# Kernel tuning notes

Measured on AMD Instinct MI355X. Metric: run time of the kernel, lower is better.

## Reference

```python
import jax, jax.numpy as jnp
import numpy as np

N = 100000      # nodes
E = 1600000     # edges (avg degree 16)
D_IN, D_H, D_OUT = 128, 128, 64
NORM_SCALE = 1.0
EPS = 1e-6


def setup_inputs() -> dict:
    key = jax.random.key(0)
    ks = jax.random.split(key, 9)
    x = jax.random.normal(ks[0], (N, D_IN), dtype=jnp.float32)
    edge_index = jax.random.randint(ks[1], (2, E), 0, N, dtype=jnp.int32)
    edge_weight = jax.random.uniform(ks[2], (E,), dtype=jnp.float32)
    # GraphConv = Linear then spmm(adj, .); Glorot-ish init for weights
    W0 = jax.random.normal(ks[3], (D_IN, D_H), dtype=jnp.float32) / np.float32(np.sqrt(D_IN))
    b0 = jnp.zeros((D_H,), jnp.float32)
    W1 = jax.random.normal(ks[4], (D_H, D_H), dtype=jnp.float32) / np.float32(np.sqrt(D_H))
    b1 = jnp.zeros((D_H,), jnp.float32)
    Wout = jax.random.normal(ks[5], (D_H, D_OUT), dtype=jnp.float32) / np.float32(np.sqrt(D_H))
    bout = jnp.zeros((D_OUT,), jnp.float32)
    return {"x": x, "edge_index": edge_index, "edge_weight": edge_weight,
            "W0": W0, "b0": b0, "W1": W1, "b1": b1, "Wout": Wout, "bout": bout}


def _pair_norm(h):
    # PairNorm mode 'PN': center columns, divide by sqrt(mean squared row norm)
    h = h - jnp.mean(h, axis=0, keepdims=True)
    rownorm_mean = jnp.sqrt(EPS + jnp.mean(jnp.sum(h * h, axis=1)))
    return NORM_SCALE * h / rownorm_mean


def reference(x, edge_index, edge_weight, W0, b0, W1, b1, Wout, bout):
    src = edge_index[0]
    dst = edge_index[1]

    def graph_conv(h, W, b):
        h = h @ W + b                              # [N, d_out]
        msg = edge_weight[:, None] * h[src]        # [E, d_out] gather
        return jax.ops.segment_sum(msg, dst, num_segments=N)  # spmm(adj, h)

    x_old = jnp.zeros((), jnp.float32)
    for (W, b) in ((W0, b0), (W1, b1)):
        # dropout p=0 -> identity (omitted)
        h = graph_conv(x, W, b)
        h = jax.nn.relu(_pair_norm(h))
        x = h + x_old        # residual=1 -> skip every layer
        x_old = x
    return graph_conv(x, Wout, bout)
```

## Files before the change

kernel.cpp:

```cpp
#include <hip/hip_runtime.h>

#define N_NODES 100000
#define N_EDGES 1600000
#define DH 128
#define DOUT 64
#define EPS 1e-6f
#define NBINS 8
#define BINW 12500
#define NREP 64

__device__ inline unsigned bfround(float f) {
    unsigned u = __float_as_uint(f);
    return (u + 0x7fffu + ((u >> 16) & 1u)) >> 16;
}
__device__ inline unsigned pack2(float a, float b) { return bfround(a) | (bfround(b) << 16); }

template <int COLS, int PN, bool OUTBF>
__global__ __launch_bounds__(256) void gemm_kernel(const float* __restrict__ Xa,
                                                   const float* __restrict__ muA,
                                                   const float* __restrict__ invA,
                                                   const float* __restrict__ Xb,
                                                   const float* __restrict__ muB,
                                                   const float* __restrict__ invB,
                                                   const float* __restrict__ W,
                                                   const float* __restrict__ bias,
                                                   void* __restrict__ Yv, int nrows) {
    constexpr int K = 128;
    constexpr int BK = 64;
    constexpr int COLG = COLS / 8;
    constexpr int ROWG = 256 / COLG;
    constexpr int RPT = 64 / ROWG;

    __shared__ float wlds[BK * COLS];
    __shared__ float xlds[64][BK + 1];

    const int tid = threadIdx.x;
    const int row0 = blockIdx.x * 64;

    const float sA = (PN >= 1) ? invA[0] : 0.f;
    const float sB = (PN == 2) ? invB[0] : 0.f;

    const int colg = tid % COLG;
    const int rowg = tid / COLG;
    const int c0 = colg * 8;
    const int r0 = rowg * RPT;

    float acc[RPT][8];
#pragma unroll
    for (int i = 0; i < RPT; ++i)
#pragma unroll
        for (int j = 0; j < 8; ++j) acc[i][j] = 0.f;

    for (int kb = 0; kb < K; kb += BK) {
        constexpr int WVEC = BK * COLS / 4;
        for (int i = tid; i < WVEC; i += 256) {
            int kr = i / (COLS / 4);
            int c4 = i % (COLS / 4);
            reinterpret_cast<float4*>(wlds)[i] =
                reinterpret_cast<const float4*>(W)[(size_t)(kb + kr) * (COLS / 4) + c4];
        }
        for (int i = tid; i < 64 * (BK / 4); i += 256) {
            int r = i / (BK / 4);
            int c4 = i % (BK / 4);
            int col4 = kb / 4 + c4;
            float4 v = make_float4(0.f, 0.f, 0.f, 0.f);
            if (row0 + r < nrows) {
                v = reinterpret_cast<const float4*>(Xa + (size_t)(row0 + r) * K)[col4];
                if constexpr (PN >= 1) {
                    float4 m = reinterpret_cast<const float4*>(muA)[col4];
                    v.x = fmaxf((v.x - m.x) * sA, 0.f);
                    v.y = fmaxf((v.y - m.y) * sA, 0.f);
                    v.z = fmaxf((v.z - m.z) * sA, 0.f);
                    v.w = fmaxf((v.w - m.w) * sA, 0.f);
                }
                if constexpr (PN == 2) {
                    float4 v2 = reinterpret_cast<const float4*>(Xb + (size_t)(row0 + r) * K)[col4];
                    float4 m2 = reinterpret_cast<const float4*>(muB)[col4];
                    v.x += fmaxf((v2.x - m2.x) * sB, 0.f);
                    v.y += fmaxf((v2.y - m2.y) * sB, 0.f);
                    v.z += fmaxf((v2.z - m2.z) * sB, 0.f);
                    v.w += fmaxf((v2.w - m2.w) * sB, 0.f);
                }
            }
            xlds[r][c4 * 4 + 0] = v.x;
            xlds[r][c4 * 4 + 1] = v.y;
            xlds[r][c4 * 4 + 2] = v.z;
            xlds[r][c4 * 4 + 3] = v.w;
        }
        __syncthreads();

        for (int k = 0; k < BK; ++k) {
            float4 w0 = *reinterpret_cast<const float4*>(&wlds[k * COLS + c0]);
            float4 w1 = *reinterpret_cast<const float4*>(&wlds[k * COLS + c0 + 4]);
#pragma unroll
            for (int i = 0; i < RPT; ++i) {
                float xv = xlds[r0 + i][k];
                acc[i][0] += xv * w0.x;
                acc[i][1] += xv * w0.y;
                acc[i][2] += xv * w0.z;
                acc[i][3] += xv * w0.w;
                acc[i][4] += xv * w1.x;
                acc[i][5] += xv * w1.y;
                acc[i][6] += xv * w1.z;
                acc[i][7] += xv * w1.w;
            }
        }
        __syncthreads();
    }

    float bv[8];
#pragma unroll
    for (int j = 0; j < 8; ++j) bv[j] = bias[c0 + j];

#pragma unroll
    for (int i = 0; i < RPT; ++i) {
        int row = row0 + r0 + i;
        if (row < nrows) {
#pragma unroll
            for (int j = 0; j < 8; ++j) acc[i][j] += bv[j];
            if constexpr (OUTBF) {
                uint4 q;
                q.x = pack2(acc[i][0], acc[i][1]);
                q.y = pack2(acc[i][2], acc[i][3]);
                q.z = pack2(acc[i][4], acc[i][5]);
                q.w = pack2(acc[i][6], acc[i][7]);
                *reinterpret_cast<uint4*>((unsigned*)Yv + ((size_t)row * COLS + c0) / 2) = q;
            } else {
                float4 o0 = make_float4(acc[i][0], acc[i][1], acc[i][2], acc[i][3]);
                float4 o1 = make_float4(acc[i][4], acc[i][5], acc[i][6], acc[i][7]);
                float4* yp = reinterpret_cast<float4*>((float*)Yv + (size_t)row * COLS + c0);
                yp[0] = o0;
                yp[1] = o1;
            }
        }
    }
}

__global__ __launch_bounds__(256) void hist_kernel(const int* __restrict__ dst,
                                                   int* __restrict__ counts) {
    int e = blockIdx.x * blockDim.x + threadIdx.x;
    const int stride = gridDim.x * blockDim.x;
    for (; e < N_EDGES; e += stride) atomicAdd(&counts[dst[e]], 1);
}

__global__ __launch_bounds__(1024) void scan_kernel(const int* __restrict__ counts,
                                                    int* __restrict__ rowptr) {
    __shared__ int wsum[16];
    const int tid = threadIdx.x;
    const int lane = tid & 63;
    const int w = tid >> 6;
    int offset = 0;
    if (tid == 0) rowptr[0] = 0;
    for (int base = 0; base < N_NODES; base += 4096) {
        int i = base + tid * 4;
        int4 v = make_int4(0, 0, 0, 0);
        if (i < N_NODES) v = *reinterpret_cast<const int4*>(counts + i);
        int p0 = v.x, p1 = p0 + v.y, p2 = p1 + v.z, p3 = p2 + v.w;
        int incl = p3;
#pragma unroll
        for (int d = 1; d < 64; d <<= 1) {
            int t = __shfl_up(incl, d, 64);
            if (lane >= d) incl += t;
        }
        if (lane == 63) wsum[w] = incl;
        __syncthreads();
        if (w == 0 && lane < 16) {
            int t = wsum[lane];
#pragma unroll
            for (int d = 1; d < 16; d <<= 1) {
                int u = __shfl_up(t, d, 64);
                if (lane >= d) t += u;
            }
            wsum[lane] = t;
        }
        __syncthreads();
        int woff = (w == 0) ? 0 : wsum[w - 1];
        int chunk_total = wsum[15];
        int tbase = offset + woff + incl - p3;
        if (i < N_NODES) {
            rowptr[i + 1] = tbase + p0;
            rowptr[i + 2] = tbase + p1;
            rowptr[i + 3] = tbase + p2;
            rowptr[i + 4] = tbase + p3;
        }
        offset += chunk_total;
        __syncthreads();
    }
}

__global__ __launch_bounds__(256) void bucket_kernel(const int* __restrict__ src,
                                                     const int* __restrict__ dst,
                                                     const float* __restrict__ ew,
                                                     const int* __restrict__ rowptr,
                                                     int* __restrict__ fill,
                                                     int2* __restrict__ em) {
    const int myBin = blockIdx.x & (NBINS - 1);
    const int lo = myBin * BINW;
    const int hi = lo + BINW;
    int e = (blockIdx.x >> 3) * 256 + threadIdx.x;
    const int stride = (gridDim.x >> 3) * 256;
    for (; e < N_EDGES; e += stride) {
        int d = dst[e];
        if (d >= lo && d < hi) {
            int pos = atomicAdd(&fill[d], 1);
            em[rowptr[d] + pos] = make_int2(src[e], __float_as_int(ew[e]));
        }
    }
}

__global__ __launch_bounds__(256) void agg128b_kernel(const unsigned* __restrict__ Hb,
                                                      const int* __restrict__ rowptr,
                                                      const int2* __restrict__ em,
                                                      float* __restrict__ B,
                                                      float* __restrict__ cs_part,
                                                      float* __restrict__ ss_part) {
    __shared__ float cs[4][128];
    __shared__ float ssw[4];
    const int wv = threadIdx.x >> 6;
    const int lane = threadIdx.x & 63;
    const int node = blockIdx.x * 4 + wv;
    const int beg = rowptr[node];
    const int end = rowptr[node + 1];
    float2 acc = make_float2(0.f, 0.f);
    for (int c = beg; c < end; c += 64) {
        int2 m = (c + lane < end) ? em[c + lane] : make_int2(0, 0);
        const int cnt = min(64, end - c);
        int k = 0;
        for (; k + 4 <= cnt; k += 4) {
#pragma unroll
            for (int j = 0; j < 4; ++j) {
                int s = __shfl(m.x, k + j, 64);
                float w = __int_as_float(__shfl(m.y, k + j, 64));
                unsigned u = Hb[(size_t)s * 64 + lane];
                acc.x += w * __uint_as_float(u << 16);
                acc.y += w * __uint_as_float(u & 0xffff0000u);
            }
        }
        for (; k < cnt; ++k) {
            int s = __shfl(m.x, k, 64);
            float w = __int_as_float(__shfl(m.y, k, 64));
            unsigned u = Hb[(size_t)s * 64 + lane];
            acc.x += w * __uint_as_float(u << 16);
            acc.y += w * __uint_as_float(u & 0xffff0000u);
        }
    }
    reinterpret_cast<float2*>(B + (size_t)node * DH)[lane] = acc;

    cs[wv][lane * 2] = acc.x;
    cs[wv][lane * 2 + 1] = acc.y;
    float sq = acc.x * acc.x + acc.y * acc.y;
#pragma unroll
    for (int off = 32; off; off >>= 1) sq += __shfl_down(sq, off, 64);
    if (lane == 0) ssw[wv] = sq;
    __syncthreads();
    const int rep = blockIdx.x & (NREP - 1);
    if (threadIdx.x < 128) {
        float s = cs[0][threadIdx.x] + cs[1][threadIdx.x] + cs[2][threadIdx.x] + cs[3][threadIdx.x];
        atomicAdd(&cs_part[rep * 128 + threadIdx.x], s);
    }
    if (threadIdx.x == 0) atomicAdd(&ss_part[rep], ssw[0] + ssw[1] + ssw[2] + ssw[3]);
}

__global__ __launch_bounds__(256) void agg64_kernel(const float* __restrict__ H,
                                                    const int* __restrict__ rowptr,
                                                    const int2* __restrict__ em,
                                                    float* __restrict__ out) {
    const int node = blockIdx.x * 4 + (threadIdx.x >> 6);
    const int lane = threadIdx.x & 63;
    const int beg = rowptr[node];
    const int end = rowptr[node + 1];
    float acc = 0.f;
    for (int c = beg; c < end; c += 64) {
        int2 m = (c + lane < end) ? em[c + lane] : make_int2(0, 0);
        const int cnt = min(64, end - c);
        int k = 0;
        for (; k + 4 <= cnt; k += 4) {
#pragma unroll
            for (int j = 0; j < 4; ++j) {
                int s = __shfl(m.x, k + j, 64);
                float w = __int_as_float(__shfl(m.y, k + j, 64));
                acc += w * H[(size_t)s * DOUT + lane];
            }
        }
        for (; k < cnt; ++k) {
            int s = __shfl(m.x, k, 64);
            float w = __int_as_float(__shfl(m.y, k, 64));
            acc += w * H[(size_t)s * DOUT + lane];
        }
    }
    out[(size_t)node * DOUT + lane] = acc;
}

__global__ void finalize_stats(const float* __restrict__ cs_part,
                               const float* __restrict__ ss_part, float* __restrict__ mu,
                               float* __restrict__ inv) {
    const int t = threadIdx.x;
    float m = 0.f;
    for (int r = 0; r < NREP; ++r) m += cs_part[r * 128 + t];
    float mean = m / (float)N_NODES;
    mu[t] = mean;
    float v = mean * mean;
    __shared__ float partl[2];
    __shared__ float sstot;
#pragma unroll
    for (int off = 32; off; off >>= 1) v += __shfl_down(v, off, 64);
    if ((t & 63) == 0) partl[t >> 6] = v;
    float ss = (t < NREP) ? ss_part[t] : 0.f;
#pragma unroll
    for (int off = 32; off; off >>= 1) ss += __shfl_down(ss, off, 64);
    if (t == 0) sstot = ss;
    __syncthreads();
    if (t == 0) {
        float musq = partl[0] + partl[1];
        float s = (sstot - (float)N_NODES * musq) / (float)N_NODES;
        inv[0] = rsqrtf(EPS + s);
    }
}

extern "C" void kernel_launch(void* const* d_in, const int* in_sizes, int n_in,
                              void* d_out, int out_size, void* d_ws, size_t ws_size,
                              hipStream_t stream) {
    const float* x = (const float*)d_in[0];
    const int* edge_index = (const int*)d_in[1];
    const float* ew = (const float*)d_in[2];
    const float* W0 = (const float*)d_in[3];
    const float* b0 = (const float*)d_in[4];
    const float* W1 = (const float*)d_in[5];
    const float* b1 = (const float*)d_in[6];
    const float* Wout = (const float*)d_in[7];
    const float* bout = (const float*)d_in[8];

    const int* src = edge_index;
    const int* dst = edge_index + N_EDGES;
    float* out = (float*)d_out;

    float* base = (float*)d_ws;
    unsigned* Hb = (unsigned*)base;
    float* HOUT = base;
    float* B1 = base + (size_t)N_NODES * 64;
    float* B2 = B1 + (size_t)N_NODES * DH;
    int2* em = (int2*)(B2 + (size_t)N_NODES * DH);
    int* counts = (int*)(em + N_EDGES);
    int* fill = counts + N_NODES;
    int* rowptr = fill + N_NODES;
    size_t soff = (size_t)(rowptr + N_NODES + 1 - (int*)base);
    soff = (soff + 3) & ~(size_t)3;
    float* stats = base + soff;
    float* cs_part1 = stats;
    float* ss_part1 = cs_part1 + NREP * 128;
    float* cs_part2 = ss_part1 + NREP;
    float* ss_part2 = cs_part2 + NREP * 128;
    float* mu1 = ss_part2 + NREP;
    float* inv1 = mu1 + 128;
    float* mu2 = inv1 + 4;
    float* inv2 = mu2 + 128;

    const int gemm_grid = (N_NODES + 63) / 64;
    const int agg_grid = N_NODES / 4;

    hipMemsetAsync(counts, 0, (size_t)2 * N_NODES * sizeof(int), stream);
    hipMemsetAsync(stats, 0, (size_t)2 * (NREP * 128 + NREP) * sizeof(float), stream);

    hist_kernel<<<2048, 256, 0, stream>>>(dst, counts);
    scan_kernel<<<1, 1024, 0, stream>>>(counts, rowptr);
    bucket_kernel<<<2048, 256, 0, stream>>>(src, dst, ew, rowptr, fill, em);

    gemm_kernel<128, 0, true><<<gemm_grid, 256, 0, stream>>>(
        x, nullptr, nullptr, nullptr, nullptr, nullptr, W0, b0, Hb, N_NODES);
    agg128b_kernel<<<agg_grid, 256, 0, stream>>>(Hb, rowptr, em, B1, cs_part1, ss_part1);
    finalize_stats<<<1, 128, 0, stream>>>(cs_part1, ss_part1, mu1, inv1);

    gemm_kernel<128, 1, true><<<gemm_grid, 256, 0, stream>>>(
        B1, mu1, inv1, nullptr, nullptr, nullptr, W1, b1, Hb, N_NODES);
    agg128b_kernel<<<agg_grid, 256, 0, stream>>>(Hb, rowptr, em, B2, cs_part2, ss_part2);
    finalize_stats<<<1, 128, 0, stream>>>(cs_part2, ss_part2, mu2, inv2);

    gemm_kernel<64, 2, false><<<gemm_grid, 256, 0, stream>>>(
        B2, mu2, inv2, B1, mu1, inv1, Wout, bout, HOUT, N_NODES);
    agg64_kernel<<<agg_grid, 256, 0, stream>>>(HOUT, rowptr, em, out);
}
```

Baseline: 615.2 us.

## Store GEMM outputs in column-sliced layout and aggregate per slice for cache locality

```diff
diff --git a/kernel.cpp b/kernel.cpp
--- a/kernel.cpp
+++ b/kernel.cpp
@@ -124,13 +124,14 @@
                 q.y = pack2(acc[i][2], acc[i][3]);
                 q.z = pack2(acc[i][4], acc[i][5]);
                 q.w = pack2(acc[i][6], acc[i][7]);
-                *reinterpret_cast<uint4*>((unsigned*)Yv + ((size_t)row * COLS + c0) / 2) = q;
+                size_t uidx = (size_t)(c0 >> 4) * ((size_t)N_NODES * 8) + (size_t)row * 8 +
+                              ((c0 >> 1) & 7);
+                *reinterpret_cast<uint4*>((unsigned*)Yv + uidx) = q;
             } else {
-                float4 o0 = make_float4(acc[i][0], acc[i][1], acc[i][2], acc[i][3]);
-                float4 o1 = make_float4(acc[i][4], acc[i][5], acc[i][6], acc[i][7]);
-                float4* yp = reinterpret_cast<float4*>((float*)Yv + (size_t)row * COLS + c0);
-                yp[0] = o0;
-                yp[1] = o1;
+                size_t fidx = (size_t)(c0 >> 3) * ((size_t)N_NODES * 8) + (size_t)row * 8;
+                float4* yp = reinterpret_cast<float4*>((float*)Yv + fidx);
+                yp[0] = make_float4(acc[i][0], acc[i][1], acc[i][2], acc[i][3]);
+                yp[1] = make_float4(acc[i][4], acc[i][5], acc[i][6], acc[i][7]);
             }
         }
     }
@@ -208,87 +209,89 @@
     }
 }
 
-__global__ __launch_bounds__(256) void agg128b_kernel(const unsigned* __restrict__ Hb,
-                                                      const int* __restrict__ rowptr,
-                                                      const int2* __restrict__ em,
-                                                      float* __restrict__ B,
-                                                      float* __restrict__ cs_part,
-                                                      float* __restrict__ ss_part) {
-    __shared__ float cs[4][128];
+template <bool BF16H, bool STATS>
+__global__ __launch_bounds__(256) void agg_sliced(const void* __restrict__ Hv,
+                                                  const int* __restrict__ rowptr,
+                                                  const int2* __restrict__ em,
+                                                  float* __restrict__ Bout,
+                                                  float* __restrict__ cs_part,
+                                                  float* __restrict__ ss_part) {
+    __shared__ float cs[4][16];
     __shared__ float ssw[4];
+    const int slice = blockIdx.x & 7;
+    const int grp = blockIdx.x >> 3;
     const int wv = threadIdx.x >> 6;
     const int lane = threadIdx.x & 63;
-    const int node = blockIdx.x * 4 + wv;
-    const int beg = rowptr[node];
-    const int end = rowptr[node + 1];
-    float2 acc = make_float2(0.f, 0.f);
-    for (int c = beg; c < end; c += 64) {
-        int2 m = (c + lane < end) ? em[c + lane] : make_int2(0, 0);
-        const int cnt = min(64, end - c);
-        int k = 0;
-        for (; k + 4 <= cnt; k += 4) {
-#pragma unroll
-            for (int j = 0; j < 4; ++j) {
-                int s = __shfl(m.x, k + j, 64);
-                float w = __int_as_float(__shfl(m.y, k + j, 64));
-                unsigned u = Hb[(size_t)s * 64 + lane];
-                acc.x += w * __uint_as_float(u << 16);
-                acc.y += w * __uint_as_float(u & 0xffff0000u);
-            }
-        }
-        for (; k < cnt; ++k) {
-            int s = __shfl(m.x, k, 64);
-            float w = __int_as_float(__shfl(m.y, k, 64));
-            unsigned u = Hb[(size_t)s * 64 + lane];
-            acc.x += w * __uint_as_float(u << 16);
-            acc.y += w * __uint_as_float(u & 0xffff0000u);
-        }
-    }
-    reinterpret_cast<float2*>(B + (size_t)node * DH)[lane] = acc;
-
-    cs[wv][lane * 2] = acc.x;
-    cs[wv][lane * 2 + 1] = acc.y;
-    float sq = acc.x * acc.x + acc.y * acc.y;
-#pragma unroll
-    for (int off = 32; off; off >>= 1) sq += __shfl_down(sq, off, 64);
-    if (lane == 0) ssw[wv] = sq;
-    __syncthreads();
-    const int rep = blockIdx.x & (NREP - 1);
-    if (threadIdx.x < 128) {
-        float s = cs[0][threadIdx.x] + cs[1][threadIdx.x] + cs[2][threadIdx.x] + cs[3][threadIdx.x];
-        atomicAdd(&cs_part[rep * 128 + threadIdx.x], s);
-    }
-    if (threadIdx.x == 0) atomicAdd(&ss_part[rep], ssw[0] + ssw[1] + ssw[2] + ssw[3]);
-}
-
-__global__ __launch_bounds__(256) void agg64_kernel(const float* __restrict__ H,
-                                                    const int* __restrict__ rowptr,
-                                                    const int2* __restrict__ em,
-                                                    float* __restrict__ out) {
-    const int node = blockIdx.x * 4 + (threadIdx.x >> 6);
-    const int lane = threadIdx.x & 63;
-    const int beg = rowptr[node];
-    const int end = rowptr[node + 1];
-    float acc = 0.f;
-    for (int c = beg; c < end; c += 64) {
-        int2 m = (c + lane < end) ? em[c + lane] : make_int2(0, 0);
-        const int cnt = min(64, end - c);
-        int k = 0;
-        for (; k + 4 <= cnt; k += 4) {
-#pragma unroll
-            for (int j = 0; j < 4; ++j) {
-                int s = __shfl(m.x, k + j, 64);
-                float w = __int_as_float(__shfl(m.y, k + j, 64));
-                acc += w * H[(size_t)s * DOUT + lane];
-            }
-        }
-        for (; k < cnt; ++k) {
-            int s = __shfl(m.x, k, 64);
-            float w = __int_as_float(__shfl(m.y, k, 64));
-            acc += w * H[(size_t)s * DOUT + lane];
-        }
-    }
-    out[(size_t)node * DOUT + lane] = acc;
+    const int g = lane >> 3;
+    const int f = lane & 7;
+    const unsigned* __restrict__ hpu =
+        (const unsigned*)Hv + (size_t)slice * ((size_t)N_NODES * 8);
+    const float* __restrict__ hpf = (const float*)Hv + (size_t)slice * ((size_t)N_NODES * 8);
+
+    float csx = 0.f, csy = 0.f, ssacc = 0.f;
+
+#pragma unroll
+    for (int nn = 0; nn < 2; ++nn) {
+        const int node = grp * 8 + nn * 4 + wv;
+        const int beg = rowptr[node];
+        const int end = rowptr[node + 1];
+        float ax = 0.f, ay = 0.f;
+        for (int c = beg; c < end; c += 64) {
+            int2 m = (c + lane < end) ? em[c + lane] : make_int2(0, 0);
+            const int cnt = min(64, end - c);
+            for (int j = 0; j < cnt; j += 8) {
+                int s = __shfl(m.x, j + g, 64);
+                float w = __int_as_float(__shfl(m.y, j + g, 64));
+                if constexpr (BF16H) {
+                    unsigned u = hpu[(size_t)s * 8 + f];
+                    ax += w * __uint_as_float(u << 16);
+                    ay += w * __uint_as_float(u & 0xffff0000u);
+                } else {
+                    ax += w * hpf[(size_t)s * 8 + f];
+                }
+            }
+        }
+        ax += __shfl_xor(ax, 8, 64);
+        ax += __shfl_xor(ax, 16, 64);
+        ax += __shfl_xor(ax, 32, 64);
+        if constexpr (BF16H) {
+            ay += __shfl_xor(ay, 8, 64);
+            ay += __shfl_xor(ay, 16, 64);
+            ay += __shfl_xor(ay, 32, 64);
+        }
+        if (lane < 8) {
+            if constexpr (BF16H) {
+                reinterpret_cast<float2*>(Bout + (size_t)node * DH + slice * 16)[f] =
+                    make_float2(ax, ay);
+            } else {
+                Bout[(size_t)node * DOUT + slice * 8 + f] = ax;
+            }
+            if constexpr (STATS) {
+                csx += ax;
+                csy += ay;
+                ssacc += ax * ax + ay * ay;
+            }
+        }
+    }
+
+    if constexpr (STATS) {
+        ssacc += __shfl_xor(ssacc, 1, 64);
+        ssacc += __shfl_xor(ssacc, 2, 64);
+        ssacc += __shfl_xor(ssacc, 4, 64);
+        if (lane < 8) {
+            cs[wv][f * 2] = csx;
+            cs[wv][f * 2 + 1] = csy;
+        }
+        if (lane == 0) ssw[wv] = ssacc;
+        __syncthreads();
+        const int rep = grp & (NREP - 1);
+        if (threadIdx.x < 16) {
+            float s =
+                cs[0][threadIdx.x] + cs[1][threadIdx.x] + cs[2][threadIdx.x] + cs[3][threadIdx.x];
+            atomicAdd(&cs_part[rep * 128 + slice * 16 + threadIdx.x], s);
+        }
+        if (threadIdx.x == 0) atomicAdd(&ss_part[rep], ssw[0] + ssw[1] + ssw[2] + ssw[3]);
+    }
 }
 
 __global__ void finalize_stats(const float* __restrict__ cs_part,
@@ -356,7 +359,7 @@
     float* inv2 = mu2 + 128;
 
     const int gemm_grid = (N_NODES + 63) / 64;
-    const int agg_grid = N_NODES / 4;
+    const int agg_grid = (N_NODES / 8) * 8;
 
     hipMemsetAsync(counts, 0, (size_t)2 * N_NODES * sizeof(int), stream);
     hipMemsetAsync(stats, 0, (size_t)2 * (NREP * 128 + NREP) * sizeof(float), stream);
@@ -367,15 +370,16 @@
 
     gemm_kernel<128, 0, true><<<gemm_grid, 256, 0, stream>>>(
         x, nullptr, nullptr, nullptr, nullptr, nullptr, W0, b0, Hb, N_NODES);
-    agg128b_kernel<<<agg_grid, 256, 0, stream>>>(Hb, rowptr, em, B1, cs_part1, ss_part1);
+    agg_sliced<true, true><<<agg_grid, 256, 0, stream>>>(Hb, rowptr, em, B1, cs_part1, ss_part1);
     finalize_stats<<<1, 128, 0, stream>>>(cs_part1, ss_part1, mu1, inv1);
 
     gemm_kernel<128, 1, true><<<gemm_grid, 256, 0, stream>>>(
         B1, mu1, inv1, nullptr, nullptr, nullptr, W1, b1, Hb, N_NODES);
-    agg128b_kernel<<<agg_grid, 256, 0, stream>>>(Hb, rowptr, em, B2, cs_part2, ss_part2);
+    agg_sliced<true, true><<<agg_grid, 256, 0, stream>>>(Hb, rowptr, em, B2, cs_part2, ss_part2);
     finalize_stats<<<1, 128, 0, stream>>>(cs_part2, ss_part2, mu2, inv2);
 
     gemm_kernel<64, 2, false><<<gemm_grid, 256, 0, stream>>>(
         B2, mu2, inv2, B1, mu1, inv1, Wout, bout, HOUT, N_NODES);
-    agg64_kernel<<<agg_grid, 256, 0, stream>>>(HOUT, rowptr, em, out);
-}
+    agg_sliced<false, false><<<agg_grid, 256, 0, stream>>>(HOUT, rowptr, em, out, nullptr,
+                                                           nullptr);
+}
```

Result: slower. 1.269 ms (+106.2%).
